# Kernel tuning notes

Measured on AMD Instinct MI355X. Metric: run time of the kernel, lower is better.

## Reference

```python
import jax, jax.numpy as jnp
import numpy as np

EPS = 1e-5
N_NODES = 100000
N_EDGES = 1600000
IN_F, HID_F, OUT_F = 128, 128, 64


def setup_inputs() -> dict:
    key = jax.random.key(0)
    ks = jax.random.split(key, 8)
    def xavier(k, fan_in, fan_out):
        lim = float(np.sqrt(6.0 / (fan_in + fan_out)))
        return jax.random.uniform(k, (fan_in, fan_out), jnp.float32, -lim, lim)
    return {
        "features": jax.random.normal(ks[0], (N_NODES, IN_F), jnp.float32),
        "src": jax.random.randint(ks[1], (N_EDGES,), 0, N_NODES, jnp.int64 if jax.config.jax_enable_x64 else jnp.int32),
        "dst": jax.random.randint(ks[2], (N_EDGES,), 0, N_NODES, jnp.int64 if jax.config.jax_enable_x64 else jnp.int32),
        "W_self1": xavier(ks[3], IN_F, HID_F),
        "W_neigh1": xavier(ks[4], IN_F, HID_F),
        "b1": jnp.zeros((HID_F,), jnp.float32),
        "gamma1": jnp.ones((HID_F,), jnp.float32),
        "beta1": jnp.zeros((HID_F,), jnp.float32),
        "W_self2": xavier(ks[5], HID_F, OUT_F),
        "W_neigh2": xavier(ks[6], HID_F, OUT_F),
        "b2": jnp.zeros((OUT_F,), jnp.float32),
        "gamma2": jnp.ones((OUT_F,), jnp.float32),
        "beta2": jnp.zeros((OUT_F,), jnp.float32),
    }


def _sage_conv(h, src, dst, W_self, W_neigh, b, n_nodes):
    # mean aggregation of source-node features onto destination nodes
    agg = jax.ops.segment_sum(h[src], dst, num_segments=n_nodes)   # [N, d]
    deg = jax.ops.segment_sum(jnp.ones_like(dst, dtype=h.dtype), dst, num_segments=n_nodes)
    h_neigh = agg / jnp.maximum(deg, 1.0)[:, None]                  # zero-degree -> 0
    return h @ W_self + h_neigh @ W_neigh + b


def _batchnorm(h, gamma, beta):
    # training-mode BatchNorm1d: batch stats over node dim, biased variance
    mu = jnp.mean(h, axis=0)
    var = jnp.mean(jnp.square(h - mu), axis=0)
    return (h - mu) * jax.lax.rsqrt(var + EPS) * gamma + beta


def reference(features, src, dst, W_self1, W_neigh1, b1, gamma1, beta1,
              W_self2, W_neigh2, b2, gamma2, beta2):
    n = features.shape[0]
    h = _sage_conv(features, src, dst, W_self1, W_neigh1, b1, n)
    h = jax.nn.relu(_batchnorm(h, gamma1, beta1))
    h = _sage_conv(h, src, dst, W_self2, W_neigh2, b2, n)
    return _batchnorm(h, gamma2, beta2)
```

## Files before the change

### kernel.cpp

```cpp
#include <hip/hip_runtime.h>

#define EPS_BN 1e-5f
#define BINSHIFT 9
#define BINW 512
#define P_EPB 8192
#define LDS_CAP 10240
#define NREP 32

typedef __attribute__((ext_vector_type(8))) short short8;
typedef __attribute__((ext_vector_type(4))) float f32x4;

__device__ __forceinline__ unsigned short f2bf(float x) {
    unsigned int u = __float_as_uint(x);
    u += 0x7fffu + ((u >> 16) & 1u);
    return (unsigned short)(u >> 16);
}
__device__ __forceinline__ float bf2f(unsigned short h) {
    return __uint_as_float(((unsigned int)h) << 16);
}
__device__ __forceinline__ float bflo(unsigned u) { return __uint_as_float(u << 16); }
__device__ __forceinline__ float bfhi(unsigned u) { return __uint_as_float(u & 0xffff0000u); }

__device__ __forceinline__ void scan512(int* a, int t) {
    for (int off = 1; off < 512; off <<= 1) {
        int v = (t >= off) ? a[t - off] : 0;
        __syncthreads();
        a[t] += v;
        __syncthreads();
    }
}
__device__ __forceinline__ void scan256(int* a, int t) {
    for (int off = 1; off < 256; off <<= 1) {
        int v = (t >= off) ? a[t - off] : 0;
        __syncthreads();
        a[t] += v;
        __syncthreads();
    }
}

__global__ __launch_bounds__(256) void prep_kernel(
    const float* __restrict__ Ws1, const float* __restrict__ Wn1,
    const float* __restrict__ Ws2, const float* __restrict__ Wn2,
    unsigned short* __restrict__ W1f, unsigned short* __restrict__ W2f,
    const int* __restrict__ dst, int* __restrict__ counts, int E, int NB, int wB) {
    int tid = threadIdx.x;
    if (blockIdx.x < wB) {
        int i = blockIdx.x * 256 + tid;
        if (i < 128 * 256) {
            int j = i & 7, L = (i >> 3) & 63, c = (i >> 9) & 15, kk = i >> 13;
            int k = kk * 32 + (L >> 4) * 8 + j;
            int col = c * 16 + (L & 15);
            float v = (col < 128) ? Ws1[k * 128 + col] : Wn1[k * 128 + (col - 128)];
            W1f[i] = f2bf(v);
        } else {
            int idx = i - 128 * 256;
            if (idx < 128 * 128) {
                int j = idx & 7, L = (idx >> 3) & 63, c = (idx >> 9) & 7, kk = idx >> 12;
                int k = kk * 32 + (L >> 4) * 8 + j;
                int col = c * 16 + (L & 15);
                float v = (col < 64) ? Ws2[k * 64 + col] : Wn2[k * 64 + (col - 64)];
                W2f[idx] = f2bf(v);
            }
        }
    } else {
        __shared__ int hist[512];
        int blk = blockIdx.x - wB;
        int e0 = blk * P_EPB, e1 = min(e0 + P_EPB, E);
        for (int b = tid; b < 512; b += 256) hist[b] = 0;
        __syncthreads();
        for (int e = e0 + tid; e < e1; e += 256) atomicAdd(&hist[dst[e] >> BINSHIFT], 1);
        __syncthreads();
        for (int b = tid; b < NB; b += 256) counts[blk * NB + b] = hist[b];
    }
}

__global__ __launch_bounds__(256) void p2a(const int* __restrict__ counts,
                                           int* __restrict__ segrel,
                                           int* __restrict__ tot, int NB, int NBLK) {
    __shared__ int s[256];
    int b = blockIdx.x, t = threadIdx.x;
    int v = (t < NBLK) ? counts[t * NB + b] : 0;
    s[t] = v;
    __syncthreads();
    scan256(s, t);
    if (t < NBLK) segrel[t * NB + b] = s[t] - v;
    if (t == 255) tot[b] = s[255];
}

__global__ __launch_bounds__(512) void p3_scatter(const int* __restrict__ src,
                                                  const int* __restrict__ dst,
                                                  const int* __restrict__ segrel,
                                                  const int* __restrict__ tot,
                                                  unsigned* __restrict__ epack,
                                                  int E, int NB) {
    __shared__ unsigned lp[P_EPB];
    __shared__ int hist[512];
    __shared__ int sBase[513];
    __shared__ int cursor[512];
    __shared__ int bbase[512];
    int t = threadIdx.x;
    int blk = blockIdx.x;
    int e0 = blk * P_EPB, e1 = min(e0 + P_EPB, E), m = e1 - e0;
    int tv = (t < NB) ? tot[t] : 0;
    bbase[t] = tv;
    __syncthreads();
    scan512(bbase, t);
    bbase[t] -= tv;
    hist[t] = 0;
    __syncthreads();
    for (int e = e0 + t; e < e1; e += 512) atomicAdd(&hist[dst[e] >> BINSHIFT], 1);
    __syncthreads();
    int h = hist[t];
    scan512(hist, t);
    int excl = hist[t] - h;
    sBase[t] = excl;
    cursor[t] = excl;
    if (t == 0) sBase[512] = m;
    __syncthreads();
    for (int e = e0 + t; e < e1; e += 512) {
        int d = dst[e];
        int pos = atomicAdd(&cursor[d >> BINSHIFT], 1);
        lp[pos] = ((unsigned)src[e] << BINSHIFT) | ((unsigned)d & (BINW - 1));
    }
    __syncthreads();
    for (int i = t; i < m; i += 512) {
        int lo = 0, hi = NB;
        while (hi - lo > 1) {
            int mid = (lo + hi) >> 1;
            if (sBase[mid] <= i) lo = mid; else hi = mid;
        }
        epack[bbase[lo] + segrel[blk * NB + lo] + (i - sBase[lo])] = lp[i];
    }
}

__global__ __launch_bounds__(512) void p4_csr(const unsigned* __restrict__ epack,
                                              const int* __restrict__ tot,
                                              int* __restrict__ row_start,
                                              int* __restrict__ cntg,
                                              float* __restrict__ inv_deg,
                                              int* __restrict__ csr_src, int N, int NB) {
    __shared__ int ncnt[512];
    __shared__ int cursor[512];
    __shared__ int bb[512];
    __shared__ int lsrc[LDS_CAP];
    int t = threadIdx.x;
    int b = blockIdx.x;
    int tv = (t < NB) ? tot[t] : 0;
    bb[t] = tv;
    __syncthreads();
    scan512(bb, t);
    int e1 = bb[b];
    int e0 = bb[b] - tot[b];
    int m = e1 - e0;
    int nbase = b << BINSHIFT;
    int nn = min(N - nbase, BINW);
    ncnt[t] = 0;
    __syncthreads();
    for (int i = e0 + t; i < e1; i += 512)
        atomicAdd(&ncnt[epack[i] & (BINW - 1)], 1);
    __syncthreads();
    int c = ncnt[t];
    scan512(ncnt, t);
    int excl = ncnt[t] - c;
    if (t < nn) {
        int node = nbase + t;
        row_start[node] = e0 + excl;
        cntg[node] = c;
        inv_deg[node] = 1.0f / fmaxf((float)c, 1.0f);
    }
    cursor[t] = excl;
    __syncthreads();
    for (int i = e0 + t; i < e1; i += 512) {
        unsigned v = epack[i];
        int pos = atomicAdd(&cursor[v & (BINW - 1)], 1);
        if (pos < LDS_CAP) lsrc[pos] = (int)(v >> BINSHIFT);
    }
    __syncthreads();
    int mm = min(m, LDS_CAP);
    for (int i = t; i < mm; i += 512) csr_src[e0 + i] = lsrc[i];
}

template <int MT, int MSELF, bool SELFBF, bool FUSEBN, bool AFP32>
__global__ __launch_bounds__(256) void gemm_dual(const unsigned short* __restrict__ Ab,
                                                 const float* __restrict__ Af,
                                                 const unsigned short* __restrict__ Wf,
                                                 float* __restrict__ YselfF,
                                                 unsigned short* __restrict__ YselfB,
                                                 unsigned short* __restrict__ Ynb, int N,
                                                 const float* __restrict__ sums,
                                                 const float* __restrict__ gamma,
                                                 const float* __restrict__ beta,
                                                 float invN) {
    constexpr int K = 128;
    constexpr int NCT = MT / 16;
    constexpr int KS = K / 32;
    constexpr int MNB = MT - MSELF;
    __shared__ unsigned short Bl[KS * NCT * 64 * 8];
    __shared__ float ssc[128], ssh[128];

    for (int i = threadIdx.x; i < KS * NCT * 64; i += 256)
        ((short8*)Bl)[i] = ((const short8*)Wf)[i];
    if (FUSEBN && threadIdx.x < 128) {
        int c = threadIdx.x;
        float su = 0.f, sq = 0.f;
        for (int r = 0; r < NREP; r++) {
            su += sums[r * 256 + c];
            sq += sums[r * 256 + 128 + c];
        }
        float mu = su * invN;
        float var = sq * invN - mu * mu;
        float sc = gamma[c] * rsqrtf(var + EPS_BN);
        ssc[c] = sc;
        ssh[c] = beta[c] - mu * sc;
    }
    __syncthreads();

    int wv = threadIdx.x >> 6, lane = threadIdx.x & 63;
    int row0 = blockIdx.x * 128 + wv * 32;
    int m = lane & 15, quad = lane >> 4;

    short8 afrag[2][KS];
#pragma unroll
    for (int t = 0; t < 2; t++) {
        int arow = row0 + t * 16 + m;
        if (arow >= N) arow = N - 1;
#pragma unroll
        for (int kk = 0; kk < KS; kk++) {
            short8 raw;
            if (AFP32) {
                const float* ap = Af + (size_t)arow * K + quad * 8 + kk * 32;
                f32x4 a = *(const f32x4*)ap;
                f32x4 b = *(const f32x4*)(ap + 4);
#pragma unroll
                for (int j = 0; j < 4; j++) {
                    raw[j] = (short)f2bf(a[j]);
                    raw[4 + j] = (short)f2bf(b[j]);
                }
            } else {
                raw = *(const short8*)(Ab + (size_t)arow * K + quad * 8 + kk * 32);
            }
            if (FUSEBN) {
#pragma unroll
                for (int j = 0; j < 8; j++) {
                    int c = kk * 32 + quad * 8 + j;
                    float f = bf2f((unsigned short)raw[j]) * ssc[c] + ssh[c];
                    raw[j] = (short)f2bf(fmaxf(f, 0.f));
                }
            }
            afrag[t][kk] = raw;
        }
    }

    f32x4 acc[2][NCT];
#pragma unroll
    for (int t = 0; t < 2; t++)
        for (int c = 0; c < NCT; c++)
            for (int j = 0; j < 4; j++) acc[t][c][j] = 0.f;

#pragma unroll
    for (int kk = 0; kk < KS; kk++) {
#pragma unroll
        for (int c = 0; c < NCT; c++) {
            short8 bfrag = *(const short8*)&Bl[((kk * NCT + c) * 64 + lane) * 8];
#pragma unroll
            for (int t = 0; t < 2; t++)
                acc[t][c] = __builtin_amdgcn_mfma_f32_16x16x32_bf16(afrag[t][kk], bfrag,
                                                                    acc[t][c], 0, 0, 0);
        }
    }

#pragma unroll
    for (int t = 0; t < 2; t++) {
#pragma unroll
        for (int c = 0; c < NCT; c++) {
            int colg = c * 16 + m;
#pragma unroll
            for (int r = 0; r < 4; r++) {
                int row = row0 + t * 16 + quad * 4 + r;
                if (row < N) {
                    float v = acc[t][c][r];
                    if (colg < MSELF) {
                        if (SELFBF)
                            YselfB[(size_t)row * MSELF + colg] = f2bf(v);
                        else
                            YselfF[(size_t)row * MSELF + colg] = v;
                    } else {
                        Ynb[(size_t)row * MNB + (colg - MSELF)] = f2bf(v);
                    }
                }
            }
        }
    }
}

__global__ __launch_bounds__(256) void agg_row128(const unsigned int* __restrict__ Sb,
                                                  const unsigned int* __restrict__ T,
                                                  const int* __restrict__ row_start,
                                                  const int* __restrict__ cnt,
                                                  const float* __restrict__ inv_deg,
                                                  const int* __restrict__ csr_src,
                                                  const float* __restrict__ bias,
                                                  unsigned int* __restrict__ Out,
                                                  float* __restrict__ sums,
                                                  int N, int totalWaves) {
    int wv = threadIdx.x >> 6, lane = threadIdx.x & 63;
    int c = lane * 2;
    float bs0 = bias[c], bs1 = bias[c + 1];
    float S0 = 0.f, S1 = 0.f, Q0 = 0.f, Q1 = 0.f;
    for (int n = blockIdx.x * 4 + wv; n < N; n += totalWaves) {
        int start = row_start[n];
        int ec = cnt[n];
        float inv = inv_deg[n];
        float a0 = 0.f, a1 = 0.f;
        int e = 0;
        for (; e + 7 < ec; e += 8) {
            int i0 = csr_src[start + e];
            int i1 = csr_src[start + e + 1];
            int i2 = csr_src[start + e + 2];
            int i3 = csr_src[start + e + 3];
            int i4 = csr_src[start + e + 4];
            int i5 = csr_src[start + e + 5];
            int i6 = csr_src[start + e + 6];
            int i7 = csr_src[start + e + 7];
            unsigned u0 = T[(size_t)i0 * 64 + lane];
            unsigned u1 = T[(size_t)i1 * 64 + lane];
            unsigned u2 = T[(size_t)i2 * 64 + lane];
            unsigned u3 = T[(size_t)i3 * 64 + lane];
            unsigned u4 = T[(size_t)i4 * 64 + lane];
            unsigned u5 = T[(size_t)i5 * 64 + lane];
            unsigned u6 = T[(size_t)i6 * 64 + lane];
            unsigned u7 = T[(size_t)i7 * 64 + lane];
            a0 += bflo(u0) + bflo(u1) + bflo(u2) + bflo(u3) +
                  bflo(u4) + bflo(u5) + bflo(u6) + bflo(u7);
            a1 += bfhi(u0) + bfhi(u1) + bfhi(u2) + bfhi(u3) +
                  bfhi(u4) + bfhi(u5) + bfhi(u6) + bfhi(u7);
        }
        for (; e < ec; e++) {
            unsigned u0 = T[(size_t)csr_src[start + e] * 64 + lane];
            a0 += bflo(u0);
            a1 += bfhi(u0);
        }
        unsigned su = Sb[(size_t)n * 64 + lane];
        float h0 = bflo(su) + a0 * inv + bs0;
        float h1 = bfhi(su) + a1 * inv + bs1;
        Out[(size_t)n * 64 + lane] = (unsigned)f2bf(h0) | ((unsigned)f2bf(h1) << 16);
        S0 += h0; Q0 += h0 * h0;
        S1 += h1; Q1 += h1 * h1;
    }
    __shared__ float ls[256];
    ls[threadIdx.x] = 0.f;
    __syncthreads();
    atomicAdd(&ls[c], S0);
    atomicAdd(&ls[c + 1], S1);
    atomicAdd(&ls[128 + c], Q0);
    atomicAdd(&ls[129 + c], Q1);
    __syncthreads();
    float* dstS = sums + (size_t)(blockIdx.x & (NREP - 1)) * 256;
    atomicAdd(&dstS[threadIdx.x], ls[threadIdx.x]);
}

__global__ __launch_bounds__(256) void agg_row64(const unsigned int* __restrict__ T,
                                                 const int* __restrict__ row_start,
                                                 const int* __restrict__ cnt,
                                                 const float* __restrict__ inv_deg,
                                                 const int* __restrict__ csr_src,
                                                 const float* __restrict__ bias,
                                                 float* Self, float* __restrict__ sums,
                                                 int N, int totalHalf) {
    int wv = threadIdx.x >> 6, L = threadIdx.x & 63;
    int g = L >> 5, h = L & 31;
    int c = h * 2;
    float bs0 = bias[c], bs1 = bias[c + 1];
    float S0 = 0.f, S1 = 0.f, Q0 = 0.f, Q1 = 0.f;
    for (int n = (blockIdx.x * 4 + wv) * 2 + g; n < N; n += totalHalf) {
        int start = row_start[n];
        int ec = cnt[n];
        float inv = inv_deg[n];
        float a0 = 0.f, a1 = 0.f;
        int e = 0;
        for (; e + 3 < ec; e += 4) {
            int i0 = csr_src[start + e];
            int i1 = csr_src[start + e + 1];
            int i2 = csr_src[start + e + 2];
            int i3 = csr_src[start + e + 3];
            unsigned u0 = T[(size_t)i0 * 32 + h];
            unsigned u1 = T[(size_t)i1 * 32 + h];
            unsigned u2 = T[(size_t)i2 * 32 + h];
            unsigned u3 = T[(size_t)i3 * 32 + h];
            a0 += bflo(u0) + bflo(u1) + bflo(u2) + bflo(u3);
            a1 += bfhi(u0) + bfhi(u1) + bfhi(u2) + bfhi(u3);
        }
        for (; e < ec; e++) {
            unsigned u0 = T[(size_t)csr_src[start + e] * 32 + h];
            a0 += bflo(u0);
            a1 += bfhi(u0);
        }
        size_t off = (size_t)n * 64 + c;
        float h0 = Self[off] + a0 * inv + bs0;
        float h1 = Self[off + 1] + a1 * inv + bs1;
        Self[off] = h0;
        Self[off + 1] = h1;
        S0 += h0; Q0 += h0 * h0;
        S1 += h1; Q1 += h1 * h1;
    }
    __shared__ float ls[128];
    if (threadIdx.x < 128) ls[threadIdx.x] = 0.f;
    __syncthreads();
    atomicAdd(&ls[c], S0);
    atomicAdd(&ls[c + 1], S1);
    atomicAdd(&ls[64 + c], Q0);
    atomicAdd(&ls[65 + c], Q1);
    __syncthreads();
    if (threadIdx.x < 128) {
        float* dstS = sums + (size_t)(blockIdx.x & (NREP - 1)) * 128;
        atomicAdd(&dstS[threadIdx.x], ls[threadIdx.x]);
    }
}

__global__ __launch_bounds__(256) void bn_apply_f64(float* H, const float* __restrict__ sums,
                                                    const float* __restrict__ gamma,
                                                    const float* __restrict__ beta,
                                                    int N, float invN) {
    __shared__ float ss[128];
    int tid = threadIdx.x;
    if (tid < 64) {
        float su = 0.f, sq = 0.f;
        for (int r = 0; r < NREP; r++) {
            su += sums[r * 128 + tid];
            sq += sums[r * 128 + 64 + tid];
        }
        float mu = su * invN;
        float var = sq * invN - mu * mu;
        float sc = gamma[tid] * rsqrtf(var + EPS_BN);
        ss[tid] = sc;
        ss[64 + tid] = beta[tid] - mu * sc;
    }
    __syncthreads();
    int total4 = N * 16;
    float4* H4 = (float4*)H;
    for (int i = blockIdx.x * 256 + threadIdx.x; i < total4; i += 256 * gridDim.x) {
        int c0 = (i * 4) & 63;
        float4 v = H4[i];
        float4 sc = *(const float4*)&ss[c0];
        float4 sh = *(const float4*)&ss[64 + c0];
        v.x = v.x * sc.x + sh.x;
        v.y = v.y * sc.y + sh.y;
        v.z = v.z * sc.z + sh.z;
        v.w = v.w * sc.w + sh.w;
        H4[i] = v;
    }
}

extern "C" void kernel_launch(void* const* d_in, const int* in_sizes, int n_in,
                              void* d_out, int out_size, void* d_ws, size_t ws_size,
                              hipStream_t stream) {
    const float* X = (const float*)d_in[0];
    const int* src = (const int*)d_in[1];
    const int* dst = (const int*)d_in[2];
    const float* Wself1 = (const float*)d_in[3];
    const float* Wneigh1 = (const float*)d_in[4];
    const float* b1 = (const float*)d_in[5];
    const float* g1 = (const float*)d_in[6];
    const float* be1 = (const float*)d_in[7];
    const float* Wself2 = (const float*)d_in[8];
    const float* Wneigh2 = (const float*)d_in[9];
    const float* b2 = (const float*)d_in[10];
    const float* g2 = (const float*)d_in[11];
    const float* be2 = (const float*)d_in[12];
    float* out = (float*)d_out;

    const int N = in_sizes[0] / 128;
    const int E = in_sizes[1];
    const int NB = (N + BINW - 1) >> BINSHIFT;
    const int NBLK = (E + P_EPB - 1) / P_EPB;

    char* p = (char*)d_ws;
    auto carve = [&](size_t bytes) {
        char* r = p;
        p += (bytes + 255) & ~(size_t)255;
        return r;
    };
    float* sums1 = (float*)carve((size_t)NREP * 256 * 4);
    float* sums2 = (float*)carve((size_t)NREP * 128 * 4);
    size_t zero_bytes = (size_t)(p - (char*)d_ws);
    int* counts = (int*)carve((size_t)NBLK * NB * 4);
    int* segrel = (int*)carve((size_t)NBLK * NB * 4);
    int* tot = (int*)carve((size_t)NB * 4);
    unsigned* epack = (unsigned*)carve((size_t)E * 4);
    int* csr_src = (int*)carve((size_t)E * 4);
    int* row_start = (int*)carve((size_t)N * 4);
    int* cntg = (int*)carve((size_t)N * 4);
    float* inv_deg = (float*)carve((size_t)N * 4);
    unsigned short* W1f = (unsigned short*)carve(128 * 256 * 2);
    unsigned short* W2f = (unsigned short*)carve(128 * 128 * 2);
    unsigned short* bufS = (unsigned short*)carve((size_t)N * 128 * 2);
    unsigned short* tab = (unsigned short*)carve((size_t)N * 128 * 2);
    unsigned short* h1b = (unsigned short*)carve((size_t)N * 128 * 2);

    hipMemsetAsync(d_ws, 0, zero_bytes, stream);

    const int wB = 192;
    const float invN = 1.0f / (float)N;
    prep_kernel<<<wB + NBLK, 256, 0, stream>>>(Wself1, Wneigh1, Wself2, Wneigh2, W1f, W2f,
                                               dst, counts, E, NB, wB);
    p2a<<<NB, 256, 0, stream>>>(counts, segrel, tot, NB, NBLK);
    p3_scatter<<<NBLK, 512, 0, stream>>>(src, dst, segrel, tot, epack, E, NB);
    p4_csr<<<NB, 512, 0, stream>>>(epack, tot, row_start, cntg, inv_deg, csr_src, N, NB);

    int ggrid = (N + 127) / 128;
    gemm_dual<256, 128, true, false, true><<<ggrid, 256, 0, stream>>>(
        nullptr, X, W1f, nullptr, bufS, tab, N, nullptr, nullptr, nullptr, 0.f);
    agg_row128<<<2048, 256, 0, stream>>>(
        (const unsigned int*)bufS, (const unsigned int*)tab, row_start, cntg, inv_deg,
        csr_src, b1, (unsigned int*)h1b, sums1, N, 8192);

    gemm_dual<128, 64, false, true, false><<<ggrid, 256, 0, stream>>>(
        h1b, nullptr, W2f, out, nullptr, tab, N, sums1, g1, be1, invN);
    agg_row64<<<2048, 256, 0, stream>>>(
        (const unsigned int*)tab, row_start, cntg, inv_deg, csr_src, b2, out, sums2,
        N, 16384);
    bn_apply_f64<<<2048, 256, 0, stream>>>(out, sums2, g2, be2, N, invN);
}
```

Baseline: 354.2 us.

## Load edge indices once per wave, broadcast via readlane, prefetch next row metadata

Both aggregation kernels now load up to 64 CSR source indices in one coalesced vector load per wave and broadcast each index with readlane, replacing per-edge scalar index loads that depended on one another. Row metadata and the first index chunk for the next node are prefetched while the current node is processed, and the gathers are unrolled to 16 or 8 loads to keep more requests in flight. agg_row64 changes from two nodes per wave to one node per wave, with the two half-waves splitting that node's edges and combining through a cross-lane shuffle. This adds more register pressure and wasted tail loads on low-degree rows.

New measurement: 354.4 us. Within noise of the previous version (+0.1%).

```diff
diff --git a/kernel.cpp b/kernel.cpp
--- a/kernel.cpp
+++ b/kernel.cpp
@@ -307,40 +307,76 @@
     int c = lane * 2;
     float bs0 = bias[c], bs1 = bias[c + 1];
     float S0 = 0.f, S1 = 0.f, Q0 = 0.f, Q1 = 0.f;
-    for (int n = blockIdx.x * 4 + wv; n < N; n += totalWaves) {
-        int start = row_start[n];
-        int ec = cnt[n];
-        float inv = inv_deg[n];
+
+    int n = blockIdx.x * 4 + wv;
+    int pStart = 0, pEc = 0, pIv = 0;
+    float pInv = 0.f;
+    if (n < N) {
+        pStart = row_start[n];
+        pEc = cnt[n];
+        pInv = inv_deg[n];
+        if (pEc > 0) pIv = csr_src[pStart + min(lane, min(pEc, 64) - 1)];
+    }
+    for (; n < N; n += totalWaves) {
+        int start = pStart, ec = pEc, iv = pIv;
+        float inv = pInv;
+        unsigned su = Sb[(size_t)n * 64 + lane];
+        int n2 = n + totalWaves;
+        if (n2 < N) {
+            pStart = row_start[n2];
+            pEc = cnt[n2];
+            pInv = inv_deg[n2];
+            if (pEc > 0) pIv = csr_src[pStart + min(lane, min(pEc, 64) - 1)];
+        }
         float a0 = 0.f, a1 = 0.f;
-        int e = 0;
-        for (; e + 7 < ec; e += 8) {
-            int i0 = csr_src[start + e];
-            int i1 = csr_src[start + e + 1];
-            int i2 = csr_src[start + e + 2];
-            int i3 = csr_src[start + e + 3];
-            int i4 = csr_src[start + e + 4];
-            int i5 = csr_src[start + e + 5];
-            int i6 = csr_src[start + e + 6];
-            int i7 = csr_src[start + e + 7];
-            unsigned u0 = T[(size_t)i0 * 64 + lane];
-            unsigned u1 = T[(size_t)i1 * 64 + lane];
-            unsigned u2 = T[(size_t)i2 * 64 + lane];
-            unsigned u3 = T[(size_t)i3 * 64 + lane];
-            unsigned u4 = T[(size_t)i4 * 64 + lane];
-            unsigned u5 = T[(size_t)i5 * 64 + lane];
-            unsigned u6 = T[(size_t)i6 * 64 + lane];
-            unsigned u7 = T[(size_t)i7 * 64 + lane];
-            a0 += bflo(u0) + bflo(u1) + bflo(u2) + bflo(u3) +
-                  bflo(u4) + bflo(u5) + bflo(u6) + bflo(u7);
-            a1 += bfhi(u0) + bfhi(u1) + bfhi(u2) + bfhi(u3) +
-                  bfhi(u4) + bfhi(u5) + bfhi(u6) + bfhi(u7);
-        }
-        for (; e < ec; e++) {
-            unsigned u0 = T[(size_t)csr_src[start + e] * 64 + lane];
-            a0 += bflo(u0);
-            a1 += bfhi(u0);
-        }
-        unsigned su = Sb[(size_t)n * 64 + lane];
+        for (int base = 0; base < ec; base += 64) {
+            int ecc = min(ec - base, 64);
+            if (base) iv = csr_src[start + base + min(lane, ecc - 1)];
+            int e = 0;
+            for (; e + 16 <= ecc; e += 16) {
+                unsigned u[16];
+#pragma unroll
+                for (int j = 0; j < 16; j++) {
+                    int s = __builtin_amdgcn_readlane(iv, e + j);
+                    u[j] = T[(size_t)s * 64 + lane];
+                }
+#pragma unroll
+                for (int j = 0; j < 16; j++) {
+                    a0 += bflo(u[j]);
+                    a1 += bfhi(u[j]);
+                }
+            }
+            if (e + 8 <= ecc) {
+                unsigned u[8];
+#pragma unroll
+                for (int j = 0; j < 8; j++) {
+                    int s = __builtin_amdgcn_readlane(iv, e + j);
+                    u[j] = T[(size_t)s * 64 + lane];
+                }
+#pragma unroll
+                for (int j = 0; j < 8; j++) {
+                    a0 += bflo(u[j]);
+                    a1 += bfhi(u[j]);
+                }
+                e += 8;
+            }
+            if (e < ecc) {
+                int r = ecc - e;
+                unsigned u[8];
+#pragma unroll
+                for (int j = 0; j < 8; j++) {
+                    int s = __builtin_amdgcn_readlane(iv, min(e + j, ecc - 1));
+                    u[j] = T[(size_t)s * 64 + lane];
+                }
+#pragma unroll
+                for (int j = 0; j < 8; j++) {
+                    if (j < r) {
+                        a0 += bflo(u[j]);
+                        a1 += bfhi(u[j]);
+                    }
+                }
+            }
+        }
         float h0 = bflo(su) + a0 * inv + bs0;
         float h1 = bfhi(su) + a1 * inv + bs1;
         Out[(size_t)n * 64 + lane] = (unsigned)f2bf(h0) | ((unsigned)f2bf(h1) << 16);
@@ -366,50 +402,88 @@
                                                  const int* __restrict__ csr_src,
                                                  const float* __restrict__ bias,
                                                  float* Self, float* __restrict__ sums,
-                                                 int N, int totalHalf) {
-    int wv = threadIdx.x >> 6, L = threadIdx.x & 63;
-    int g = L >> 5, h = L & 31;
+                                                 int N, int totalWaves) {
+    int wv = threadIdx.x >> 6, lane = threadIdx.x & 63;
+    int g = lane >> 5, h = lane & 31;
     int c = h * 2;
     float bs0 = bias[c], bs1 = bias[c + 1];
     float S0 = 0.f, S1 = 0.f, Q0 = 0.f, Q1 = 0.f;
-    for (int n = (blockIdx.x * 4 + wv) * 2 + g; n < N; n += totalHalf) {
-        int start = row_start[n];
-        int ec = cnt[n];
+
+    int n = blockIdx.x * 4 + wv;
+    int pStart = 0, pEc = 0, pIv = 0;
+    if (n < N) {
+        pStart = row_start[n];
+        pEc = cnt[n];
+        if (pEc > 0) pIv = csr_src[pStart + min(lane, min(pEc, 64) - 1)];
+    }
+    for (; n < N; n += totalWaves) {
+        int start = pStart, ec = pEc, iv = pIv;
         float inv = inv_deg[n];
+        int n2 = n + totalWaves;
+        if (n2 < N) {
+            pStart = row_start[n2];
+            pEc = cnt[n2];
+            if (pEc > 0) pIv = csr_src[pStart + min(lane, min(pEc, 64) - 1)];
+        }
         float a0 = 0.f, a1 = 0.f;
-        int e = 0;
-        for (; e + 3 < ec; e += 4) {
-            int i0 = csr_src[start + e];
-            int i1 = csr_src[start + e + 1];
-            int i2 = csr_src[start + e + 2];
-            int i3 = csr_src[start + e + 3];
-            unsigned u0 = T[(size_t)i0 * 32 + h];
-            unsigned u1 = T[(size_t)i1 * 32 + h];
-            unsigned u2 = T[(size_t)i2 * 32 + h];
-            unsigned u3 = T[(size_t)i3 * 32 + h];
-            a0 += bflo(u0) + bflo(u1) + bflo(u2) + bflo(u3);
-            a1 += bfhi(u0) + bfhi(u1) + bfhi(u2) + bfhi(u3);
-        }
-        for (; e < ec; e++) {
-            unsigned u0 = T[(size_t)csr_src[start + e] * 32 + h];
-            a0 += bflo(u0);
-            a1 += bfhi(u0);
-        }
-        size_t off = (size_t)n * 64 + c;
-        float h0 = Self[off] + a0 * inv + bs0;
-        float h1 = Self[off + 1] + a1 * inv + bs1;
-        Self[off] = h0;
-        Self[off + 1] = h1;
-        S0 += h0; Q0 += h0 * h0;
-        S1 += h1; Q1 += h1 * h1;
+        for (int base = 0; base < ec; base += 64) {
+            int ecc = min(ec - base, 64);
+            if (base) iv = csr_src[start + base + min(lane, ecc - 1)];
+            int e = 0;
+            for (; e + 8 <= ecc; e += 8) {
+                unsigned u[4];
+#pragma unroll
+                for (int j = 0; j < 4; j++) {
+                    int s0 = __builtin_amdgcn_readlane(iv, e + 2 * j);
+                    int s1 = __builtin_amdgcn_readlane(iv, e + 2 * j + 1);
+                    int sg = g ? s1 : s0;
+                    u[j] = T[(size_t)sg * 32 + h];
+                }
+#pragma unroll
+                for (int j = 0; j < 4; j++) {
+                    a0 += bflo(u[j]);
+                    a1 += bfhi(u[j]);
+                }
+            }
+            if (e < ecc) {
+                int r = ecc - e;
+                unsigned u[4];
+#pragma unroll
+                for (int j = 0; j < 4; j++) {
+                    int s0 = __builtin_amdgcn_readlane(iv, min(e + 2 * j, ecc - 1));
+                    int s1 = __builtin_amdgcn_readlane(iv, min(e + 2 * j + 1, ecc - 1));
+                    int sg = g ? s1 : s0;
+                    u[j] = T[(size_t)sg * 32 + h];
+                }
+#pragma unroll
+                for (int j = 0; j < 4; j++) {
+                    bool ok = (2 * j + g) < r;
+                    a0 += ok ? bflo(u[j]) : 0.f;
+                    a1 += ok ? bfhi(u[j]) : 0.f;
+                }
+            }
+        }
+        a0 += __shfl_xor(a0, 32);
+        a1 += __shfl_xor(a1, 32);
+        if (g == 0) {
+            size_t off = (size_t)n * 64 + c;
+            float h0 = Self[off] + a0 * inv + bs0;
+            float h1 = Self[off + 1] + a1 * inv + bs1;
+            Self[off] = h0;
+            Self[off + 1] = h1;
+            S0 += h0; Q0 += h0 * h0;
+            S1 += h1; Q1 += h1 * h1;
+        }
     }
     __shared__ float ls[128];
     if (threadIdx.x < 128) ls[threadIdx.x] = 0.f;
     __syncthreads();
-    atomicAdd(&ls[c], S0);
-    atomicAdd(&ls[c + 1], S1);
-    atomicAdd(&ls[64 + c], Q0);
-    atomicAdd(&ls[65 + c], Q1);
+    if (g == 0) {
+        atomicAdd(&ls[c], S0);
+        atomicAdd(&ls[c + 1], S1);
+        atomicAdd(&ls[64 + c], Q0);
+        atomicAdd(&ls[65 + c], Q1);
+    }
     __syncthreads();
     if (threadIdx.x < 128) {
         float* dstS = sums + (size_t)(blockIdx.x & (NREP - 1)) * 128;
@@ -518,6 +592,6 @@
         h1b, nullptr, W2f, out, nullptr, tab, N, sums1, g1, be1, invN);
     agg_row64<<<2048, 256, 0, stream>>>(
         (const unsigned int*)tab, row_start, cntg, inv_deg, csr_src, b2, out, sums2,
-        N, 16384);
+        N, 8192);
     bn_apply_f64<<<2048, 256, 0, stream>>>(out, sums2, g2, be2, N, invN);
 }
```

## Sort CSR edges by source chunk and aggregate chunk-by-chunk with cooperative prefetch

Applied to the files above, without the earlier changes.

The CSR build now sub-sorts each node's edges by source-node chunk (8192 rows) and records per-node segment offsets for each chunk. Both aggregation kernels walk the source chunks in lockstep, with every wave handling 14 nodes per chunk, so that at any moment all waves gather from a small L2-resident slice of the feature table. Each wave also prefetches its share of the next chunk into cache with vector loads. The aim is to turn random gathers over the whole table into cache-local ones, at the cost of more complex control flow, an extra seg array, per-chunk overhead for low-degree nodes, and the removal of the LDS staging in the CSR scatter.

New measurement: 545.4 us. 54.0% more time.

```diff
diff --git a/kernel.cpp b/kernel.cpp
--- a/kernel.cpp
+++ b/kernel.cpp
@@ -4,8 +4,10 @@
 #define BINSHIFT 9
 #define BINW 512
 #define P_EPB 8192
-#define LDS_CAP 10240
 #define NREP 32
+#define CHSH 13
+#define SEGSTRIDE 16
+#define NPW 14
 
 typedef __attribute__((ext_vector_type(8))) short short8;
 typedef __attribute__((ext_vector_type(4))) float f32x4;
@@ -138,46 +140,54 @@
                                               int* __restrict__ row_start,
                                               int* __restrict__ cntg,
                                               float* __restrict__ inv_deg,
-                                              int* __restrict__ csr_src, int N, int NB) {
-    __shared__ int ncnt[512];
-    __shared__ int cursor[512];
+                                              int* __restrict__ csr_src,
+                                              int* __restrict__ seg, int N, int NB) {
+    __shared__ int kc[8192];
     __shared__ int bb[512];
-    __shared__ int lsrc[LDS_CAP];
-    int t = threadIdx.x;
-    int b = blockIdx.x;
+    __shared__ int ts[512];
+    int t = threadIdx.x, b = blockIdx.x;
     int tv = (t < NB) ? tot[t] : 0;
     bb[t] = tv;
     __syncthreads();
     scan512(bb, t);
-    int e1 = bb[b];
-    int e0 = bb[b] - tot[b];
-    int m = e1 - e0;
+    int e1 = bb[b], e0 = e1 - tot[b];
     int nbase = b << BINSHIFT;
     int nn = min(N - nbase, BINW);
-    ncnt[t] = 0;
-    __syncthreads();
-    for (int i = e0 + t; i < e1; i += 512)
-        atomicAdd(&ncnt[epack[i] & (BINW - 1)], 1);
-    __syncthreads();
-    int c = ncnt[t];
-    scan512(ncnt, t);
-    int excl = ncnt[t] - c;
+    for (int k = t; k < 8192; k += 512) kc[k] = 0;
+    __syncthreads();
+    for (int i = e0 + t; i < e1; i += 512) {
+        unsigned v = epack[i];
+        int key = ((v & (BINW - 1)) << 4) | (int)(v >> (BINSHIFT + CHSH));
+        atomicAdd(&kc[key], 1);
+    }
+    __syncthreads();
+    int loc[16];
+    int s = 0;
+#pragma unroll
+    for (int c = 0; c < 16; c++) { loc[c] = s; s += kc[t * 16 + c]; }
+    ts[t] = s;
+    __syncthreads();
+    scan512(ts, t);
+    int nodeExcl = ts[t] - s;
     if (t < nn) {
         int node = nbase + t;
-        row_start[node] = e0 + excl;
-        cntg[node] = c;
-        inv_deg[node] = 1.0f / fmaxf((float)c, 1.0f);
-    }
-    cursor[t] = excl;
+        row_start[node] = e0 + nodeExcl;
+        cntg[node] = s;
+        inv_deg[node] = 1.0f / fmaxf((float)s, 1.0f);
+#pragma unroll
+        for (int c = 0; c < 16; c++)
+            seg[(size_t)node * SEGSTRIDE + c] = e0 + nodeExcl + loc[c];
+    }
+    __syncthreads();
+#pragma unroll
+    for (int c = 0; c < 16; c++) kc[t * 16 + c] = nodeExcl + loc[c];
     __syncthreads();
     for (int i = e0 + t; i < e1; i += 512) {
         unsigned v = epack[i];
-        int pos = atomicAdd(&cursor[v & (BINW - 1)], 1);
-        if (pos < LDS_CAP) lsrc[pos] = (int)(v >> BINSHIFT);
-    }
-    __syncthreads();
-    int mm = min(m, LDS_CAP);
-    for (int i = t; i < mm; i += 512) csr_src[e0 + i] = lsrc[i];
+        int key = ((v & (BINW - 1)) << 4) | (int)(v >> (BINSHIFT + CHSH));
+        int pos = atomicAdd(&kc[key], 1);
+        csr_src[e0 + pos] = (int)(v >> BINSHIFT);
+    }
 }
 
 template <int MT, int MSELF, bool SELFBF, bool FUSEBN, bool AFP32>
@@ -293,60 +303,122 @@
     }
 }
 
-__global__ __launch_bounds__(256) void agg_row128(const unsigned int* __restrict__ Sb,
-                                                  const unsigned int* __restrict__ T,
-                                                  const int* __restrict__ row_start,
-                                                  const int* __restrict__ cnt,
-                                                  const float* __restrict__ inv_deg,
-                                                  const int* __restrict__ csr_src,
-                                                  const float* __restrict__ bias,
-                                                  unsigned int* __restrict__ Out,
-                                                  float* __restrict__ sums,
-                                                  int N, int totalWaves) {
+__global__ __launch_bounds__(256, 7) void agg_row128_ch(
+    const unsigned int* __restrict__ Sb, const unsigned int* __restrict__ T,
+    const int* __restrict__ seg, const float* __restrict__ inv_deg,
+    const int* __restrict__ csr_src, const float* __restrict__ bias,
+    unsigned int* __restrict__ Out, float* __restrict__ sums, int N, int E) {
     int wv = threadIdx.x >> 6, lane = threadIdx.x & 63;
     int c = lane * 2;
     float bs0 = bias[c], bs1 = bias[c + 1];
     float S0 = 0.f, S1 = 0.f, Q0 = 0.f, Q1 = 0.f;
-    for (int n = blockIdx.x * 4 + wv; n < N; n += totalWaves) {
-        int start = row_start[n];
-        int ec = cnt[n];
-        float inv = inv_deg[n];
-        float a0 = 0.f, a1 = 0.f;
-        int e = 0;
-        for (; e + 7 < ec; e += 8) {
-            int i0 = csr_src[start + e];
-            int i1 = csr_src[start + e + 1];
-            int i2 = csr_src[start + e + 2];
-            int i3 = csr_src[start + e + 3];
-            int i4 = csr_src[start + e + 4];
-            int i5 = csr_src[start + e + 5];
-            int i6 = csr_src[start + e + 6];
-            int i7 = csr_src[start + e + 7];
-            unsigned u0 = T[(size_t)i0 * 64 + lane];
-            unsigned u1 = T[(size_t)i1 * 64 + lane];
-            unsigned u2 = T[(size_t)i2 * 64 + lane];
-            unsigned u3 = T[(size_t)i3 * 64 + lane];
-            unsigned u4 = T[(size_t)i4 * 64 + lane];
-            unsigned u5 = T[(size_t)i5 * 64 + lane];
-            unsigned u6 = T[(size_t)i6 * 64 + lane];
-            unsigned u7 = T[(size_t)i7 * 64 + lane];
-            a0 += bflo(u0) + bflo(u1) + bflo(u2) + bflo(u3) +
-                  bflo(u4) + bflo(u5) + bflo(u6) + bflo(u7);
-            a1 += bfhi(u0) + bfhi(u1) + bfhi(u2) + bfhi(u3) +
-                  bfhi(u4) + bfhi(u5) + bfhi(u6) + bfhi(u7);
-        }
-        for (; e < ec; e++) {
-            unsigned u0 = T[(size_t)csr_src[start + e] * 64 + lane];
-            a0 += bflo(u0);
-            a1 += bfhi(u0);
-        }
-        unsigned su = Sb[(size_t)n * 64 + lane];
-        float h0 = bflo(su) + a0 * inv + bs0;
-        float h1 = bfhi(su) + a1 * inv + bs1;
-        Out[(size_t)n * 64 + lane] = (unsigned)f2bf(h0) | ((unsigned)f2bf(h1) << 16);
-        S0 += h0; Q0 += h0 * h0;
-        S1 += h1; Q1 += h1 * h1;
-    }
+    int totalWaves = gridDim.x * 4;
+    int w = blockIdx.x * 4 + wv;
+    int wpx = (gridDim.x >> 3) * 4;
+    int wix = (blockIdx.x >> 3) * 4 + wv;
+    int nch = (N + (1 << CHSH) - 1) >> CHSH;
+    float wsum = 0.f;
+    f32x4 wb0 = {0, 0, 0, 0}, wb1 = {0, 0, 0, 0}, wb2 = {0, 0, 0, 0};
+    for (int nb = w * NPW; nb < N; nb += totalWaves * NPW) {
+        float a0[NPW], a1[NPW];
+#pragma unroll
+        for (int i = 0; i < NPW; i++) { a0[i] = 0.f; a1[i] = 0.f; }
+        {
+            int rows = min(N, 1 << CHSH);
+            int cdw = rows * 64;
+            int sdw = ((cdw + wpx - 1) / wpx + 3) & ~3;
+            long endd = (long)cdw;
+#pragma unroll
+            for (int st = 0; st < 3; st++) {
+                long ad = (long)wix * sdw + st * 256 + lane * 4;
+                if (ad + 4 > endd) ad = endd - 4;
+                f32x4 v = *(const f32x4*)((const float*)T + ad);
+                if (st == 0) wb0 = v; else if (st == 1) wb1 = v; else wb2 = v;
+            }
+        }
+        for (int cc = 0; cc < nch; cc++) {
+            wsum += wb0[0] + wb0[3] + wb1[0] + wb1[3] + wb2[0] + wb2[3];
+            int jj = lane & 15; jj = (jj < NPW) ? jj : NPW - 1;
+            int bSel = (lane >> 4) & 1;
+            long sidx = (long)min(nb + jj, N - 1) * SEGSTRIDE + cc + bSel;
+            int bv = seg[sidx];
+#pragma unroll
+            for (int gp = 0; gp < 2; gp++) {
+                int lo_[7], hi_[7], s0_[7], s1_[7];
+#pragma unroll
+                for (int k = 0; k < 7; k++) {
+                    int i = gp * 7 + k;
+                    lo_[k] = __builtin_amdgcn_readlane(bv, i);
+                    hi_[k] = __builtin_amdgcn_readlane(bv, 16 + i);
+                }
+#pragma unroll
+                for (int k = 0; k < 7; k++) {
+                    int last = max(hi_[k] - 1, 0);
+                    int i0 = min(lo_[k], last);
+                    int i1 = min(lo_[k] + 1, last);
+                    s0_[k] = csr_src[min(i0, E - 1)];
+                    s1_[k] = csr_src[min(i1, E - 1)];
+                }
+                unsigned ua[7], ub[7];
+#pragma unroll
+                for (int k = 0; k < 7; k++) {
+                    ua[k] = T[(size_t)s0_[k] * 64 + lane];
+                    ub[k] = T[(size_t)s1_[k] * 64 + lane];
+                }
+#pragma unroll
+                for (int k = 0; k < 7; k++) {
+                    int i = gp * 7 + k;
+                    bool valid = (nb + i < N);
+                    int len = hi_[k] - lo_[k];
+                    a0[i] += (valid && len >= 1) ? bflo(ua[k]) : 0.f;
+                    a1[i] += (valid && len >= 1) ? bfhi(ua[k]) : 0.f;
+                    a0[i] += (valid && len >= 2) ? bflo(ub[k]) : 0.f;
+                    a1[i] += (valid && len >= 2) ? bfhi(ub[k]) : 0.f;
+                    if (valid) {
+                        for (int e = lo_[k] + 2; e < hi_[k]; e++) {
+                            unsigned u = T[(size_t)csr_src[e] * 64 + lane];
+                            a0[i] += bflo(u);
+                            a1[i] += bfhi(u);
+                        }
+                    }
+                }
+                if (cc + 1 < nch) {
+                    int rowsN = min(N - ((cc + 1) << CHSH), 1 << CHSH);
+                    int cdw = rowsN * 64;
+                    int sdw = ((cdw + wpx - 1) / wpx + 3) & ~3;
+                    long cb = ((long)(cc + 1) << CHSH) * 64;
+                    long endd = cb + cdw;
+                    if (gp == 0) {
+#pragma unroll
+                        for (int st = 0; st < 2; st++) {
+                            long ad = cb + (long)wix * sdw + st * 256 + lane * 4;
+                            if (ad + 4 > endd) ad = endd - 4;
+                            f32x4 v = *(const f32x4*)((const float*)T + ad);
+                            if (st == 0) wb0 = v; else wb1 = v;
+                        }
+                    } else {
+                        long ad = cb + (long)wix * sdw + 2 * 256 + lane * 4;
+                        if (ad + 4 > endd) ad = endd - 4;
+                        wb2 = *(const f32x4*)((const float*)T + ad);
+                    }
+                }
+            }
+        }
+#pragma unroll
+        for (int i = 0; i < NPW; i++) {
+            int n = nb + i;
+            if (n < N) {
+                float inv = inv_deg[n];
+                unsigned su = Sb[(size_t)n * 64 + lane];
+                float h0 = bflo(su) + a0[i] * inv + bs0;
+                float h1 = bfhi(su) + a1[i] * inv + bs1;
+                Out[(size_t)n * 64 + lane] = (unsigned)f2bf(h0) | ((unsigned)f2bf(h1) << 16);
+                S0 += h0; Q0 += h0 * h0;
+                S1 += h1; Q1 += h1 * h1;
+            }
+        }
+    }
+    asm volatile("" :: "v"(wsum));
     __shared__ float ls[256];
     ls[threadIdx.x] = 0.f;
     __syncthreads();
@@ -359,57 +431,138 @@
     atomicAdd(&dstS[threadIdx.x], ls[threadIdx.x]);
 }
 
-__global__ __launch_bounds__(256) void agg_row64(const unsigned int* __restrict__ T,
-                                                 const int* __restrict__ row_start,
-                                                 const int* __restrict__ cnt,
-                                                 const float* __restrict__ inv_deg,
-                                                 const int* __restrict__ csr_src,
-                                                 const float* __restrict__ bias,
-                                                 float* Self, float* __restrict__ sums,
-                                                 int N, int totalHalf) {
-    int wv = threadIdx.x >> 6, L = threadIdx.x & 63;
-    int g = L >> 5, h = L & 31;
-    int c = h * 2;
-    float bs0 = bias[c], bs1 = bias[c + 1];
+__global__ __launch_bounds__(256, 7) void agg_row64_ch(
+    const unsigned int* __restrict__ T, const int* __restrict__ seg,
+    const float* __restrict__ inv_deg, const int* __restrict__ csr_src,
+    const float* __restrict__ bias, float* Self, float* __restrict__ sums,
+    int N, int E) {
+    int wv = threadIdx.x >> 6, lane = threadIdx.x & 63;
+    int g = lane >> 5, h = lane & 31;
+    int c2 = h * 2;
+    float bs0 = bias[c2], bs1 = bias[c2 + 1];
     float S0 = 0.f, S1 = 0.f, Q0 = 0.f, Q1 = 0.f;
-    for (int n = (blockIdx.x * 4 + wv) * 2 + g; n < N; n += totalHalf) {
-        int start = row_start[n];
-        int ec = cnt[n];
-        float inv = inv_deg[n];
-        float a0 = 0.f, a1 = 0.f;
-        int e = 0;
-        for (; e + 3 < ec; e += 4) {
-            int i0 = csr_src[start + e];
-            int i1 = csr_src[start + e + 1];
-            int i2 = csr_src[start + e + 2];
-            int i3 = csr_src[start + e + 3];
-            unsigned u0 = T[(size_t)i0 * 32 + h];
-            unsigned u1 = T[(size_t)i1 * 32 + h];
-            unsigned u2 = T[(size_t)i2 * 32 + h];
-            unsigned u3 = T[(size_t)i3 * 32 + h];
-            a0 += bflo(u0) + bflo(u1) + bflo(u2) + bflo(u3);
-            a1 += bfhi(u0) + bfhi(u1) + bfhi(u2) + bfhi(u3);
-        }
-        for (; e < ec; e++) {
-            unsigned u0 = T[(size_t)csr_src[start + e] * 32 + h];
-            a0 += bflo(u0);
-            a1 += bfhi(u0);
-        }
-        size_t off = (size_t)n * 64 + c;
-        float h0 = Self[off] + a0 * inv + bs0;
-        float h1 = Self[off + 1] + a1 * inv + bs1;
-        Self[off] = h0;
-        Self[off + 1] = h1;
-        S0 += h0; Q0 += h0 * h0;
-        S1 += h1; Q1 += h1 * h1;
-    }
+    int totalWaves = gridDim.x * 4;
+    int w = blockIdx.x * 4 + wv;
+    int wpx = (gridDim.x >> 3) * 4;
+    int wix = (blockIdx.x >> 3) * 4 + wv;
+    int nch = (N + (1 << CHSH) - 1) >> CHSH;
+    float wsum = 0.f;
+    f32x4 wb0 = {0, 0, 0, 0}, wb1 = {0, 0, 0, 0};
+    for (int nb = w * NPW; nb < N; nb += totalWaves * NPW) {
+        float a0[NPW], a1[NPW];
+#pragma unroll
+        for (int i = 0; i < NPW; i++) { a0[i] = 0.f; a1[i] = 0.f; }
+        {
+            int rows = min(N, 1 << CHSH);
+            int cdw = rows * 32;
+            int sdw = ((cdw + wpx - 1) / wpx + 3) & ~3;
+            long endd = (long)cdw;
+#pragma unroll
+            for (int st = 0; st < 2; st++) {
+                long ad = (long)wix * sdw + st * 256 + lane * 4;
+                if (ad + 4 > endd) ad = endd - 4;
+                f32x4 v = *(const f32x4*)((const float*)T + ad);
+                if (st == 0) wb0 = v; else wb1 = v;
+            }
+        }
+        for (int cc = 0; cc < nch; cc++) {
+            wsum += wb0[0] + wb0[3] + wb1[0] + wb1[3];
+            int jj = lane & 15; jj = (jj < NPW) ? jj : NPW - 1;
+            int bSel = (lane >> 4) & 1;
+            long sidx = (long)min(nb + jj, N - 1) * SEGSTRIDE + cc + bSel;
+            int bv = seg[sidx];
+#pragma unroll
+            for (int gp = 0; gp < 2; gp++) {
+                int lo_[7], hi_[7], s0_[7], s1_[7];
+#pragma unroll
+                for (int k = 0; k < 7; k++) {
+                    int i = gp * 7 + k;
+                    lo_[k] = __builtin_amdgcn_readlane(bv, i);
+                    hi_[k] = __builtin_amdgcn_readlane(bv, 16 + i);
+                }
+#pragma unroll
+                for (int k = 0; k < 7; k++) {
+                    int last = max(hi_[k] - 1, 0);
+                    int i0 = min(lo_[k], last);
+                    int i1 = min(lo_[k] + 1, last);
+                    s0_[k] = csr_src[min(i0, E - 1)];
+                    s1_[k] = csr_src[min(i1, E - 1)];
+                }
+                unsigned up[7];
+#pragma unroll
+                for (int k = 0; k < 7; k++) {
+                    int sg = g ? s1_[k] : s0_[k];
+                    up[k] = T[(size_t)sg * 32 + h];
+                }
+#pragma unroll
+                for (int k = 0; k < 7; k++) {
+                    int i = gp * 7 + k;
+                    bool valid = (nb + i < N);
+                    int len = hi_[k] - lo_[k];
+                    bool ok = valid && (len > g);
+                    a0[i] += ok ? bflo(up[k]) : 0.f;
+                    a1[i] += ok ? bfhi(up[k]) : 0.f;
+                    if (valid) {
+                        int e = lo_[k] + 2;
+                        for (; e + 2 <= hi_[k]; e += 2) {
+                            int t0 = csr_src[e], t1 = csr_src[e + 1];
+                            int sg = g ? t1 : t0;
+                            unsigned u = T[(size_t)sg * 32 + h];
+                            a0[i] += bflo(u);
+                            a1[i] += bfhi(u);
+                        }
+                        if (e < hi_[k]) {
+                            unsigned u = T[(size_t)csr_src[e] * 32 + h];
+                            a0[i] += g ? 0.f : bflo(u);
+                            a1[i] += g ? 0.f : bfhi(u);
+                        }
+                    }
+                }
+                if (cc + 1 < nch && gp == 0) {
+                    int rowsN = min(N - ((cc + 1) << CHSH), 1 << CHSH);
+                    int cdw = rowsN * 32;
+                    int sdw = ((cdw + wpx - 1) / wpx + 3) & ~3;
+                    long cb = ((long)(cc + 1) << CHSH) * 32;
+                    long endd = cb + cdw;
+#pragma unroll
+                    for (int st = 0; st < 2; st++) {
+                        long ad = cb + (long)wix * sdw + st * 256 + lane * 4;
+                        if (ad + 4 > endd) ad = endd - 4;
+                        f32x4 v = *(const f32x4*)((const float*)T + ad);
+                        if (st == 0) wb0 = v; else wb1 = v;
+                    }
+                }
+            }
+        }
+#pragma unroll
+        for (int i = 0; i < NPW; i++) {
+            int n = nb + i;
+            if (n < N) {
+                float x0 = a0[i] + __shfl_xor(a0[i], 32);
+                float x1 = a1[i] + __shfl_xor(a1[i], 32);
+                if (g == 0) {
+                    float inv = inv_deg[n];
+                    size_t off = (size_t)n * 64 + c2;
+                    float h0 = Self[off] + x0 * inv + bs0;
+                    float h1 = Self[off + 1] + x1 * inv + bs1;
+                    Self[off] = h0;
+                    Self[off + 1] = h1;
+                    S0 += h0; Q0 += h0 * h0;
+                    S1 += h1; Q1 += h1 * h1;
+                }
+            }
+        }
+    }
+    asm volatile("" :: "v"(wsum));
     __shared__ float ls[128];
     if (threadIdx.x < 128) ls[threadIdx.x] = 0.f;
     __syncthreads();
-    atomicAdd(&ls[c], S0);
-    atomicAdd(&ls[c + 1], S1);
-    atomicAdd(&ls[64 + c], Q0);
-    atomicAdd(&ls[65 + c], Q1);
+    if (g == 0) {
+        atomicAdd(&ls[c2], S0);
+        atomicAdd(&ls[c2 + 1], S1);
+        atomicAdd(&ls[64 + c2], Q0);
+        atomicAdd(&ls[65 + c2], Q1);
+    }
     __syncthreads();
     if (threadIdx.x < 128) {
         float* dstS = sums + (size_t)(blockIdx.x & (NREP - 1)) * 128;
@@ -491,6 +644,7 @@
     int* row_start = (int*)carve((size_t)N * 4);
     int* cntg = (int*)carve((size_t)N * 4);
     float* inv_deg = (float*)carve((size_t)N * 4);
+    int* seg = (int*)carve((size_t)N * SEGSTRIDE * 4);
     unsigned short* W1f = (unsigned short*)carve(128 * 256 * 2);
     unsigned short* W2f = (unsigned short*)carve(128 * 128 * 2);
     unsigned short* bufS = (unsigned short*)carve((size_t)N * 128 * 2);
@@ -505,19 +659,19 @@
                                                dst, counts, E, NB, wB);
     p2a<<<NB, 256, 0, stream>>>(counts, segrel, tot, NB, NBLK);
     p3_scatter<<<NBLK, 512, 0, stream>>>(src, dst, segrel, tot, epack, E, NB);
-    p4_csr<<<NB, 512, 0, stream>>>(epack, tot, row_start, cntg, inv_deg, csr_src, N, NB);
+    p4_csr<<<NB, 512, 0, stream>>>(epack, tot, row_start, cntg, inv_deg, csr_src, seg,
+                                   N, NB);
 
     int ggrid = (N + 127) / 128;
     gemm_dual<256, 128, true, false, true><<<ggrid, 256, 0, stream>>>(
         nullptr, X, W1f, nullptr, bufS, tab, N, nullptr, nullptr, nullptr, 0.f);
-    agg_row128<<<2048, 256, 0, stream>>>(
-        (const unsigned int*)bufS, (const unsigned int*)tab, row_start, cntg, inv_deg,
-        csr_src, b1, (unsigned int*)h1b, sums1, N, 8192);
+    agg_row128_ch<<<1792, 256, 0, stream>>>(
+        (const unsigned int*)bufS, (const unsigned int*)tab, seg, inv_deg, csr_src, b1,
+        (unsigned int*)h1b, sums1, N, E);
 
     gemm_dual<128, 64, false, true, false><<<ggrid, 256, 0, stream>>>(
         h1b, nullptr, W2f, out, nullptr, tab, N, sums1, g1, be1, invN);
-    agg_row64<<<2048, 256, 0, stream>>>(
-        (const unsigned int*)tab, row_start, cntg, inv_deg, csr_src, b2, out, sums2,
-        N, 16384);
+    agg_row64_ch<<<1792, 256, 0, stream>>>(
+        (const unsigned int*)tab, seg, inv_deg, csr_src, b2, out, sums2, N, E);
     bn_apply_f64<<<2048, 256, 0, stream>>>(out, sums2, g2, be2, N, invN);
 }
```
